# Kernel tuning notes

Hardware: AMD Instinct MI355X
Metric: run time of the kernel (lower is better)

Reference implementation:

```python
import jax, jax.numpy as jnp
import numpy as np

TIME_SHIFT_OFFSET = 288
NOTE_OFF_OFFSET = 128
VELOCITY_OFFSET = 256
MAX_REL_POS = 25
MAX_REL_TIME = 200
MAX_REL_PITCH = 128


def _last_true_pos(flag):
    # flag: (B,T) bool -> (B,T) index of most recent True at or before each position, -1 if none
    B, T = flag.shape
    pos = jnp.where(flag, jnp.arange(T)[None, :], -1)
    return jax.lax.cummax(pos, axis=1)


def time_rel_idx(tok):
    # Faithful vectorization of Head.relative_time index computation.
    B, T = tok.shape
    is_t = tok >= TIME_SHIFT_OFFSET
    vals = jnp.where(is_t, tok - TIME_SHIFT_OFFSET, 0)
    abs_t = (jnp.cumsum(vals, axis=1) + 1).astype(jnp.float32)
    last = _last_true_pos(is_t)
    cur = jnp.where(last >= 0, jnp.take_along_axis(abs_t, jnp.maximum(last, 0), axis=1), jnp.nan)
    prop = jnp.round(cur / 10.0)  # (B,T), NaN before first time token
    dist = prop[:, None, :] - prop[:, :, None]  # [b,i,j] = prop[j]-prop[i]
    idx = jnp.clip(dist, -MAX_REL_TIME, MAX_REL_TIME) + MAX_REL_TIME
    return jnp.where(jnp.isnan(idx), 0.0, idx).astype(jnp.int32)  # (B,T,T)


def pitch_rel_idx(tok):
    # Per the reference loop, note values are also written one step ahead (i-1,i,i+1),
    # so position j ends up with the note value known after step min(j+1, T-1).
    B, T = tok.shape
    is_n = tok < VELOCITY_OFFSET
    vals = (jnp.where(tok >= NOTE_OFF_OFFSET, tok - NOTE_OFF_OFFSET, tok) + 1).astype(jnp.float32)
    last = _last_true_pos(is_n)
    ff = jnp.where(last >= 0, jnp.take_along_axis(vals, jnp.maximum(last, 0), axis=1), jnp.nan)
    prop = ff[:, jnp.minimum(jnp.arange(T) + 1, T - 1)]
    dist = prop[:, None, :] - prop[:, :, None]
    idx = jnp.clip(dist, -MAX_REL_PITCH, MAX_REL_PITCH) + MAX_REL_PITCH
    return jnp.where(jnp.isnan(idx), 0.0, idx).astype(jnp.int32)  # (B,T,T)


def setup_inputs() -> dict:
    key = jax.random.key(0)
    ks = jax.random.split(key, 12)
    B, T, C, H = 2, 512, 512, 64
    x = jax.random.normal(ks[0], (B, T, C), dtype=jnp.float32)
    token_batch = jax.random.randint(ks[1], (B, T), 0, 388)
    s = C ** -0.5
    Wk = jax.random.normal(ks[2], (C, H), dtype=jnp.float32) * s
    Wq = jax.random.normal(ks[3], (C, H), dtype=jnp.float32) * s
    Wv = jax.random.normal(ks[4], (C, H), dtype=jnp.float32) * s
    e = 0.02
    Ek_pos = jax.random.normal(ks[5], (2 * MAX_REL_POS + 1, H), dtype=jnp.float32) * e
    Ev_pos = jax.random.normal(ks[6], (2 * MAX_REL_POS + 1, H), dtype=jnp.float32) * e
    Ek_time = jax.random.normal(ks[7], (2 * MAX_REL_TIME + 1, H), dtype=jnp.float32) * e
    Ev_time = jax.random.normal(ks[8], (2 * MAX_REL_TIME + 1, H), dtype=jnp.float32) * e
    Ek_pitch = jax.random.normal(ks[9], (2 * MAX_REL_PITCH + 1, H), dtype=jnp.float32) * e
    Ev_pitch = jax.random.normal(ks[10], (2 * MAX_REL_PITCH + 1, H), dtype=jnp.float32) * e
    return dict(x=x, token_batch=token_batch, Wk=Wk, Wq=Wq, Wv=Wv,
                Ek_pos=Ek_pos, Ev_pos=Ev_pos, Ek_time=Ek_time, Ev_time=Ev_time,
                Ek_pitch=Ek_pitch, Ev_pitch=Ev_pitch)


def reference(x, token_batch, Wk, Wq, Wv, Ek_pos, Ev_pos, Ek_time, Ev_time, Ek_pitch, Ev_pitch):
    B, T, C = x.shape
    q = x @ Wq  # (B,T,H)
    k = x @ Wk
    v = x @ Wv
    wei = jnp.einsum('btc,bsc->bts', q, k) * (C ** -0.5)  # (B,T,T), scaled by n_embd per source
    pos = jnp.arange(T)
    pd = jnp.clip(pos[None, :] - pos[:, None], -MAX_REL_POS, MAX_REL_POS) + MAX_REL_POS  # (T,T)
    tidx = time_rel_idx(token_batch)
    nidx = pitch_rel_idx(token_batch)
    # Note: the source einsums sum the relative embeddings over i as well (btj output).
    wei = wei + jnp.einsum('ijc,btc->btj', Ek_pos[pd], q)
    wei = wei + jnp.einsum('bijc,btc->btj', Ek_time[tidx], q)
    wei = wei + jnp.einsum('bijc,btc->btj', Ek_pitch[nidx], q)
    causal = jnp.tril(jnp.ones((T, T), dtype=bool))
    wei = jnp.where(causal[None], wei, -jnp.inf)
    wei = jax.nn.softmax(wei, axis=-1)  # dropout p=0.0
    out = wei @ v
    out = out + jnp.einsum('ijc,btj->btc', Ev_pos[pd], wei)
    out = out + jnp.einsum('bijc,btj->btc', Ev_time[tidx], wei)
    out = out + jnp.einsum('bijc,btj->btc', Ev_pitch[nidx], wei)
    return out
```

## Files before the change

### kernel.cpp

```cpp
#include <hip/hip_runtime.h>
#include <math.h>

#define B 2
#define T 512
#define C 512
#define H 64

#define SCALE 0.044194173824159216f

static __device__ __forceinline__ float qnan() { return __builtin_nanf(""); }

__global__ __launch_bounds__(64) void scan_kernel(const int* __restrict__ tok,
                                                  float* __restrict__ prop_t,
                                                  float* __restrict__ prop_p,
                                                  int* __restrict__ cntP,
                                                  int* __restrict__ meta,
                                                  float* __restrict__ tval,
                                                  int* __restrict__ tcnt) {
    int b = blockIdx.x;
    int lane = threadIdx.x;
    const int* tb = tok + b * T;

    __shared__ int tks[T];
    __shared__ float ptv[T];
    __shared__ float ff[T];
    __shared__ int hist[129];
    __shared__ int cnts[520];
    __shared__ int nanPc;

    for (int i = lane; i < T; i += 64) tks[i] = tb[i];
    for (int i = lane; i < 520; i += 64) cnts[i] = 0;
    for (int i = lane; i < 129; i += 64) hist[i] = 0;
    if (lane == 0) nanPc = 0;
    __syncthreads();

    const int p0 = lane * 8;
    unsigned long long lowmask = lane ? ((1ull << lane) - 1ull) : 0ull;

    {
        float lsum[8];
        bool lflag[8];
        float s = 0.f;
        bool f = false;
#pragma unroll
        for (int i = 0; i < 8; ++i) {
            int tk = tks[p0 + i];
            if (tk >= 288) { s += (float)(tk - 288); f = true; }
            lsum[i] = s;
            lflag[i] = f;
        }
        float inc = s;
#pragma unroll
        for (int off = 1; off < 64; off <<= 1) {
            float o = __shfl_up(inc, off);
            if (lane >= off) inc += o;
        }
        float ex = inc - s;
        unsigned long long fmask = __ballot(f);
        bool exf = (fmask & lowmask) != 0ull;
#pragma unroll
        for (int i = 0; i < 8; ++i) {
            bool have = exf | lflag[i];
            float outv = have ? rintf((ex + lsum[i] + 1.0f) / 10.0f) : qnan();
            prop_t[b * T + p0 + i] = outv;
            ptv[p0 + i] = outv;
        }
    }

    {
        float lval[8];
        bool lvalid[8];
        float cv = 0.f;
        bool cvd = false;
#pragma unroll
        for (int i = 0; i < 8; ++i) {
            int tk = tks[p0 + i];
            if (tk < 256) {
                cv = (float)((tk >= 128 ? tk - 128 : tk) + 1);
                cvd = true;
            }
            lval[i] = cv;
            lvalid[i] = cvd;
        }
        unsigned long long vmask = __ballot(cvd);
        unsigned long long lower = vmask & lowmask;
        bool exvd = lower != 0ull;
        int src = 63 - __clzll(lower | 1ull);
        float exv = __shfl(cv, src);
#pragma unroll
        for (int i = 0; i < 8; ++i) {
            bool hv = exvd | lvalid[i];
            float fv = lvalid[i] ? lval[i] : exv;
            ff[p0 + i] = hv ? fv : qnan();
        }
    }
    __syncthreads();

    for (int i = lane; i < T; i += 64) {
        float v = ff[min(i + 1, T - 1)];
        prop_p[b * T + i] = v;
        if (v == v) atomicAdd(&hist[(int)v - 1], 1);
        else atomicAdd(&nanPc, 1);
    }

    int lstart[8];
    int lcnt = 0, lnan = 0;
#pragma unroll
    for (int u = 0; u < 8; ++u) {
        int i = p0 + u;
        float cur = ptv[i];
        bool val = (cur == cur);
        bool st = false;
        if (val) {
            if (i == 0) st = true;
            else {
                float pv = ptv[i - 1];
                st = !(pv == pv) || (pv != cur);
            }
        } else lnan++;
        lstart[u] = st;
        lcnt += st;
    }
    int incs = lcnt;
#pragma unroll
    for (int off = 1; off < 64; off <<= 1) {
        int o = __shfl_up(incs, off);
        if (lane >= off) incs += o;
    }
    int base = incs - lcnt;
    int Lruns = __shfl(incs, 63);
    int tn = lnan;
#pragma unroll
    for (int off = 32; off; off >>= 1) tn += __shfl_down(tn, off);
    tn = __shfl(tn, 0);

    int s2 = base;
#pragma unroll
    for (int u = 0; u < 8; ++u) {
        int i = p0 + u;
        float cur = ptv[i];
        if (lstart[u]) { tval[b * 520 + s2] = cur; s2++; }
        if (cur == cur) atomicAdd(&cnts[s2 - 1], 1);
    }
    __syncthreads();

    for (int i = lane; i < Lruns; i += 64) tcnt[b * 520 + i] = cnts[i];
    for (int i = lane; i < 129; i += 64) cntP[b * 129 + i] = hist[i];
    if (lane == 0) {
        meta[b * 4] = Lruns;
        meta[b * 4 + 1] = tn;
        meta[b * 4 + 2] = nanPc;
    }
}

__global__ __launch_bounds__(256) void qkv_kernel(const float* __restrict__ x,
                                                  const float* __restrict__ Wq,
                                                  const float* __restrict__ Wk,
                                                  const float* __restrict__ Wv,
                                                  float* __restrict__ q,
                                                  float* __restrict__ k,
                                                  float* __restrict__ v) {
    int rg = blockIdx.x & 63;
    int m = blockIdx.x >> 6;
    int tid = threadIdx.x;
    int wave = tid >> 6;
    int lane = tid & 63;
    int g = lane >> 4;
    int c4 = lane & 15;

    const float* Wm = (m == 0) ? Wq : ((m == 1) ? Wk : Wv);
    float* Om = (m == 0) ? q : ((m == 1) ? k : v);

    __shared__ float xs[16 * C];
    const float4* xv4 = (const float4*)(x + (size_t)rg * 16 * C);
    float4* xs4 = (float4*)xs;
#pragma unroll
    for (int i = 0; i < 8; ++i) xs4[tid + 256 * i] = xv4[tid + 256 * i];
    __syncthreads();

    const float4* W4 = (const float4*)Wm;
    const float* xr = xs + (wave * 4) * C;

    float4 a0 = make_float4(0.f, 0.f, 0.f, 0.f);
    float4 a1 = a0, a2 = a0, a3 = a0;
#pragma unroll 4
    for (int u = 0; u < 128; ++u) {
        int kk = u * 4 + g;
        float4 w4 = W4[kk * 16 + c4];
        float x0 = xr[kk];
        float x1 = xr[C + kk];
        float x2 = xr[2 * C + kk];
        float x3 = xr[3 * C + kk];
        a0.x = fmaf(x0, w4.x, a0.x); a0.y = fmaf(x0, w4.y, a0.y);
        a0.z = fmaf(x0, w4.z, a0.z); a0.w = fmaf(x0, w4.w, a0.w);
        a1.x = fmaf(x1, w4.x, a1.x); a1.y = fmaf(x1, w4.y, a1.y);
        a1.z = fmaf(x1, w4.z, a1.z); a1.w = fmaf(x1, w4.w, a1.w);
        a2.x = fmaf(x2, w4.x, a2.x); a2.y = fmaf(x2, w4.y, a2.y);
        a2.z = fmaf(x2, w4.z, a2.z); a2.w = fmaf(x2, w4.w, a2.w);
        a3.x = fmaf(x3, w4.x, a3.x); a3.y = fmaf(x3, w4.y, a3.y);
        a3.z = fmaf(x3, w4.z, a3.z); a3.w = fmaf(x3, w4.w, a3.w);
    }

#pragma unroll
    for (int mask = 16; mask <= 32; mask <<= 1) {
        a0.x += __shfl_xor(a0.x, mask); a0.y += __shfl_xor(a0.y, mask);
        a0.z += __shfl_xor(a0.z, mask); a0.w += __shfl_xor(a0.w, mask);
        a1.x += __shfl_xor(a1.x, mask); a1.y += __shfl_xor(a1.y, mask);
        a1.z += __shfl_xor(a1.z, mask); a1.w += __shfl_xor(a1.w, mask);
        a2.x += __shfl_xor(a2.x, mask); a2.y += __shfl_xor(a2.y, mask);
        a2.z += __shfl_xor(a2.z, mask); a2.w += __shfl_xor(a2.w, mask);
        a3.x += __shfl_xor(a3.x, mask); a3.y += __shfl_xor(a3.y, mask);
        a3.z += __shfl_xor(a3.z, mask); a3.w += __shfl_xor(a3.w, mask);
    }

    if (g == 0) {
        size_t row0 = (size_t)(rg * 16 + wave * 4);
        ((float4*)(Om + (row0 + 0) * H))[c4] = a0;
        ((float4*)(Om + (row0 + 1) * H))[c4] = a1;
        ((float4*)(Om + (row0 + 2) * H))[c4] = a2;
        ((float4*)(Om + (row0 + 3) * H))[c4] = a3;
    }
}

__global__ __launch_bounds__(256) void relsum_kernel(
    const float* __restrict__ prop_t, const float* __restrict__ prop_p,
    const int* __restrict__ cntP, const int* __restrict__ meta,
    const float* __restrict__ tval, const int* __restrict__ tcnt,
    const float* __restrict__ Ek_pos, const float* __restrict__ Ev_pos,
    const float* __restrict__ Ek_time, const float* __restrict__ Ev_time,
    const float* __restrict__ Ek_pitch, const float* __restrict__ Ev_pitch,
    float* __restrict__ k, float* __restrict__ v) {
    int b = blockIdx.x >> 9;
    int j = blockIdx.x & 511;
    int tid = threadIdx.x;
    int wave = tid >> 6;
    int c = tid & 63;

    __shared__ float tvL[520];
    __shared__ int tcL[520];
    __shared__ int cpL[132];
    __shared__ float redK[256];
    __shared__ float redV[256];

    int L = meta[b * 4];
    int nanT = meta[b * 4 + 1];
    int nanP = meta[b * 4 + 2];
    for (int i = tid; i < L; i += 256) {
        tvL[i] = tval[b * 520 + i];
        tcL[i] = tcnt[b * 520 + i];
    }
    if (tid < 129) cpL[tid] = cntP[b * 129 + tid];
    else if (tid < 132) cpL[tid] = 0;
    __syncthreads();

    float pjt = prop_t[b * T + j];
    float pjp = prop_p[b * T + j];
    bool pvalid = (pjp == pjp);
    int ipjp = pvalid ? (int)pjp : 0;

    float aK = 0.f, aV = 0.f;

#pragma unroll 3
    for (int i = 0; i < 33; ++i) {
        int e = wave + i * 4;
        int cnt = cpL[e];
        if (cnt) {
            int idx = pvalid ? (ipjp + 127 - e) : 0;
            float fc = (float)cnt;
            aK = fmaf(fc, Ek_pitch[idx * H + c], aK);
            aV = fmaf(fc, Ev_pitch[idx * H + c], aV);
        }
    }
    if (wave == 3 && nanP) {
        float fc = (float)nanP;
        aK = fmaf(fc, Ek_pitch[c], aK);
        aV = fmaf(fc, Ev_pitch[c], aV);
    }

#pragma unroll 2
    for (int r = wave; r < L; r += 4) {
        int cnt = tcL[r];
        float dt = pjt - tvL[r];
        int idx = (dt != dt) ? 0 : (int)fminf(fmaxf(dt, -200.f), 200.f) + 200;
        float fc = (float)cnt;
        aK = fmaf(fc, Ek_time[idx * H + c], aK);
        aV = fmaf(fc, Ev_time[idx * H + c], aV);
    }
    if (wave == 1 && nanT) {
        float fc = (float)nanT;
        aK = fmaf(fc, Ek_time[c], aK);
        aV = fmaf(fc, Ev_time[c], aV);
    }

    int lo = max(-25, j - (T - 1));
    int hi = min(25, j);
    for (int d = lo + wave; d <= hi; d += 4) {
        aK += Ek_pos[(d + 25) * H + c];
        aV += Ev_pos[(d + 25) * H + c];
    }
    if (wave == 0) {
        float c50 = (float)max(j - 25, 0);
        float c0 = (float)max((T - 26) - j, 0);
        aK = fmaf(c50, Ek_pos[50 * H + c], aK);
        aK = fmaf(c0, Ek_pos[0 * H + c], aK);
        aV = fmaf(c50, Ev_pos[50 * H + c], aV);
        aV = fmaf(c0, Ev_pos[0 * H + c], aV);
    }

    redK[tid] = aK;
    redV[tid] = aV;
    __syncthreads();

    if (tid < 64) {
        float sK = redK[tid] + redK[64 + tid] + redK[128 + tid] + redK[192 + tid];
        float sV = redV[tid] + redV[64 + tid] + redV[128 + tid] + redV[192 + tid];
        size_t o = (size_t)blockIdx.x * H + tid;
        k[o] = SCALE * k[o] + sK;
        v[o] = v[o] + sV;
    }
}

__global__ __launch_bounds__(256) void attn_kernel(const float* __restrict__ q,
                                                   const float* __restrict__ kp,
                                                   const float* __restrict__ vp,
                                                   float* __restrict__ out) {
    int b = blockIdx.x >> 7;
    int g = blockIdx.x & 127;
    int tid = threadIdx.x;
    int wave = tid >> 6;
    int lane = tid & 63;

    int t = (wave < 2) ? (2 * g + wave) : (511 - 2 * g - (wave - 2));
    int ns = t + 1;

    __shared__ float kt[64 * 65];
    __shared__ float vt[64 * 64];
    __shared__ float qs[4][64];
    __shared__ float pS[4][64];

    qs[wave][lane] = q[((size_t)b * T + t) * H + lane];

    const float* kb = kp + (size_t)b * T * H;
    const float* vb = vp + (size_t)b * T * H;
    int ntiles = (512 - 2 * g + 63) / 64;

    float m = -INFINITY;
    float l = 0.f;
    float acc = 0.f;

    for (int it = 0; it < ntiles; ++it) {
        int s0 = it * 64;

#pragma unroll
        for (int i = 0; i < 4; ++i) {
            int f = i * 256 + tid;
            int r = f >> 4;
            int c0 = (f & 15) << 2;
            int sr = min(s0 + r, T - 1);
            const float4 kv = *(const float4*)(kb + (size_t)sr * H + c0);
            const float4 vv = *(const float4*)(vb + (size_t)sr * H + c0);
            kt[r * 65 + c0 + 0] = kv.x;
            kt[r * 65 + c0 + 1] = kv.y;
            kt[r * 65 + c0 + 2] = kv.z;
            kt[r * 65 + c0 + 3] = kv.w;
            *(float4*)(vt + r * 64 + c0) = vv;
        }
        __syncthreads();

        if (s0 < ns) {
            int s = s0 + lane;
            float sc = -INFINITY;
            if (s < ns) {
                const float* kr = kt + lane * 65;
                const float* qw = qs[wave];
                float d0 = 0.f, d1 = 0.f, d2 = 0.f, d3 = 0.f;
#pragma unroll
                for (int c = 0; c < 64; c += 4) {
                    d0 = fmaf(qw[c + 0], kr[c + 0], d0);
                    d1 = fmaf(qw[c + 1], kr[c + 1], d1);
                    d2 = fmaf(qw[c + 2], kr[c + 2], d2);
                    d3 = fmaf(qw[c + 3], kr[c + 3], d3);
                }
                sc = (d0 + d1) + (d2 + d3);
            }
            float mt = sc;
#pragma unroll
            for (int off = 32; off; off >>= 1) mt = fmaxf(mt, __shfl_xor(mt, off));
            float mnew = fmaxf(m, mt);
            float alpha = __expf(m - mnew);
            float p = (s < ns) ? __expf(sc - mnew) : 0.f;
            l = l * alpha + p;
            pS[wave][lane] = p;
            m = mnew;

            float a0 = 0.f, a1 = 0.f, a2 = 0.f, a3 = 0.f;
            int smax = min(64, ns - s0);
            const float* pw = pS[wave];
            int ss = 0;
            for (; ss + 4 <= smax; ss += 4) {
                a0 = fmaf(pw[ss + 0], vt[(ss + 0) * 64 + lane], a0);
                a1 = fmaf(pw[ss + 1], vt[(ss + 1) * 64 + lane], a1);
                a2 = fmaf(pw[ss + 2], vt[(ss + 2) * 64 + lane], a2);
                a3 = fmaf(pw[ss + 3], vt[(ss + 3) * 64 + lane], a3);
            }
            for (; ss < smax; ++ss)
                a0 = fmaf(pw[ss], vt[ss * 64 + lane], a0);
            acc = acc * alpha + ((a0 + a1) + (a2 + a3));
        }
        __syncthreads();
    }

    float lt = l;
#pragma unroll
    for (int off = 32; off; off >>= 1) lt += __shfl_xor(lt, off);

    out[((size_t)b * T + t) * H + lane] = acc / lt;
}

extern "C" void kernel_launch(void* const* d_in, const int* in_sizes, int n_in,
                              void* d_out, int out_size, void* d_ws, size_t ws_size,
                              hipStream_t stream) {
    const float* x        = (const float*)d_in[0];
    const int*   tok      = (const int*)d_in[1];
    const float* Wk       = (const float*)d_in[2];
    const float* Wq       = (const float*)d_in[3];
    const float* Wv       = (const float*)d_in[4];
    const float* Ek_pos   = (const float*)d_in[5];
    const float* Ev_pos   = (const float*)d_in[6];
    const float* Ek_time  = (const float*)d_in[7];
    const float* Ev_time  = (const float*)d_in[8];
    const float* Ek_pitch = (const float*)d_in[9];
    const float* Ev_pitch = (const float*)d_in[10];
    float* out = (float*)d_out;

    float* ws = (float*)d_ws;
    float* q      = ws;
    float* k      = q + B * T * H;
    float* v      = k + B * T * H;
    float* prop_t = v + B * T * H;
    float* prop_p = prop_t + B * T;
    int*   cntP   = (int*)(prop_p + B * T);
    int*   meta   = cntP + B * 129;
    float* tval   = (float*)(meta + B * 4);
    int*   tcnt   = (int*)(tval + B * 520);

    scan_kernel<<<B, 64, 0, stream>>>(tok, prop_t, prop_p, cntP, meta, tval, tcnt);
    qkv_kernel<<<3 * 64, 256, 0, stream>>>(x, Wq, Wk, Wv, q, k, v);
    relsum_kernel<<<B * T, 256, 0, stream>>>(prop_t, prop_p, cntP, meta, tval, tcnt,
                                             Ek_pos, Ev_pos, Ek_time, Ev_time,
                                             Ek_pitch, Ev_pitch, k, v);
    attn_kernel<<<B * 128, 256, 0, stream>>>(q, k, v, out);
}
```

Baseline: 131.0 us.

## Fuse token scan, QKV projection and relative-sum into one kernel

Merges three kernels (scan, qkv, relsum) into a single kernel of 256 blocks. Each block handles 4 rows: wave 0 redoes the per-batch token scan in shared memory, and waves 1-3 compute the q, k and v projections for those rows. After a barrier, each wave does the relative-embedding sum for one row with no cross-wave reduction. This removes two launches and the global round-trips for intermediates, but every block repeats the scan redundantly and each wave now walks the full pitch and time loops serially.

```diff
diff --git a/kernel.cpp b/kernel.cpp
--- a/kernel.cpp
+++ b/kernel.cpp
@@ -10,314 +10,279 @@
 
 static __device__ __forceinline__ float qnan() { return __builtin_nanf(""); }
 
-__global__ __launch_bounds__(64) void scan_kernel(const int* __restrict__ tok,
-                                                  float* __restrict__ prop_t,
-                                                  float* __restrict__ prop_p,
-                                                  int* __restrict__ cntP,
-                                                  int* __restrict__ meta,
-                                                  float* __restrict__ tval,
-                                                  int* __restrict__ tcnt) {
-    int b = blockIdx.x;
-    int lane = threadIdx.x;
-    const int* tb = tok + b * T;
-
-    __shared__ int tks[T];
-    __shared__ float ptv[T];
-    __shared__ float ff[T];
-    __shared__ int hist[129];
-    __shared__ int cnts[520];
-    __shared__ int nanPc;
-
-    for (int i = lane; i < T; i += 64) tks[i] = tb[i];
-    for (int i = lane; i < 520; i += 64) cnts[i] = 0;
-    for (int i = lane; i < 129; i += 64) hist[i] = 0;
-    if (lane == 0) nanPc = 0;
-    __syncthreads();
-
-    const int p0 = lane * 8;
-    unsigned long long lowmask = lane ? ((1ull << lane) - 1ull) : 0ull;
-
-    {
-        float lsum[8];
-        bool lflag[8];
-        float s = 0.f;
-        bool f = false;
-#pragma unroll
-        for (int i = 0; i < 8; ++i) {
-            int tk = tks[p0 + i];
-            if (tk >= 288) { s += (float)(tk - 288); f = true; }
-            lsum[i] = s;
-            lflag[i] = f;
-        }
-        float inc = s;
-#pragma unroll
-        for (int off = 1; off < 64; off <<= 1) {
-            float o = __shfl_up(inc, off);
-            if (lane >= off) inc += o;
-        }
-        float ex = inc - s;
-        unsigned long long fmask = __ballot(f);
-        bool exf = (fmask & lowmask) != 0ull;
-#pragma unroll
-        for (int i = 0; i < 8; ++i) {
-            bool have = exf | lflag[i];
-            float outv = have ? rintf((ex + lsum[i] + 1.0f) / 10.0f) : qnan();
-            prop_t[b * T + p0 + i] = outv;
-            ptv[p0 + i] = outv;
-        }
-    }
-
-    {
-        float lval[8];
-        bool lvalid[8];
-        float cv = 0.f;
-        bool cvd = false;
-#pragma unroll
-        for (int i = 0; i < 8; ++i) {
-            int tk = tks[p0 + i];
-            if (tk < 256) {
-                cv = (float)((tk >= 128 ? tk - 128 : tk) + 1);
-                cvd = true;
-            }
-            lval[i] = cv;
-            lvalid[i] = cvd;
-        }
-        unsigned long long vmask = __ballot(cvd);
-        unsigned long long lower = vmask & lowmask;
-        bool exvd = lower != 0ull;
-        int src = 63 - __clzll(lower | 1ull);
-        float exv = __shfl(cv, src);
-#pragma unroll
-        for (int i = 0; i < 8; ++i) {
-            bool hv = exvd | lvalid[i];
-            float fv = lvalid[i] ? lval[i] : exv;
-            ff[p0 + i] = hv ? fv : qnan();
-        }
-    }
-    __syncthreads();
-
-    for (int i = lane; i < T; i += 64) {
-        float v = ff[min(i + 1, T - 1)];
-        prop_p[b * T + i] = v;
-        if (v == v) atomicAdd(&hist[(int)v - 1], 1);
-        else atomicAdd(&nanPc, 1);
-    }
-
-    int lstart[8];
-    int lcnt = 0, lnan = 0;
-#pragma unroll
-    for (int u = 0; u < 8; ++u) {
-        int i = p0 + u;
-        float cur = ptv[i];
-        bool val = (cur == cur);
-        bool st = false;
-        if (val) {
-            if (i == 0) st = true;
-            else {
-                float pv = ptv[i - 1];
-                st = !(pv == pv) || (pv != cur);
-            }
-        } else lnan++;
-        lstart[u] = st;
-        lcnt += st;
-    }
-    int incs = lcnt;
-#pragma unroll
-    for (int off = 1; off < 64; off <<= 1) {
-        int o = __shfl_up(incs, off);
-        if (lane >= off) incs += o;
-    }
-    int base = incs - lcnt;
-    int Lruns = __shfl(incs, 63);
-    int tn = lnan;
-#pragma unroll
-    for (int off = 32; off; off >>= 1) tn += __shfl_down(tn, off);
-    tn = __shfl(tn, 0);
-
-    int s2 = base;
-#pragma unroll
-    for (int u = 0; u < 8; ++u) {
-        int i = p0 + u;
-        float cur = ptv[i];
-        if (lstart[u]) { tval[b * 520 + s2] = cur; s2++; }
-        if (cur == cur) atomicAdd(&cnts[s2 - 1], 1);
-    }
-    __syncthreads();
-
-    for (int i = lane; i < Lruns; i += 64) tcnt[b * 520 + i] = cnts[i];
-    for (int i = lane; i < 129; i += 64) cntP[b * 129 + i] = hist[i];
-    if (lane == 0) {
-        meta[b * 4] = Lruns;
-        meta[b * 4 + 1] = tn;
-        meta[b * 4 + 2] = nanPc;
-    }
-}
-
-__global__ __launch_bounds__(256) void qkv_kernel(const float* __restrict__ x,
-                                                  const float* __restrict__ Wq,
-                                                  const float* __restrict__ Wk,
-                                                  const float* __restrict__ Wv,
-                                                  float* __restrict__ q,
-                                                  float* __restrict__ k,
-                                                  float* __restrict__ v) {
-    int rg = blockIdx.x & 63;
-    int m = blockIdx.x >> 6;
+__global__ __launch_bounds__(256) void fused_kernel(
+    const int* __restrict__ tok, const float* __restrict__ x,
+    const float* __restrict__ Wq, const float* __restrict__ Wk,
+    const float* __restrict__ Wv,
+    const float* __restrict__ Ek_pos, const float* __restrict__ Ev_pos,
+    const float* __restrict__ Ek_time, const float* __restrict__ Ev_time,
+    const float* __restrict__ Ek_pitch, const float* __restrict__ Ev_pitch,
+    float* __restrict__ q, float* __restrict__ k, float* __restrict__ v) {
+    int bid = blockIdx.x;
+    int b = bid >> 7;
+    int j0 = (bid & 127) * 4;
     int tid = threadIdx.x;
     int wave = tid >> 6;
     int lane = tid & 63;
-    int g = lane >> 4;
-    int c4 = lane & 15;
-
-    const float* Wm = (m == 0) ? Wq : ((m == 1) ? Wk : Wv);
-    float* Om = (m == 0) ? q : ((m == 1) ? k : v);
-
-    __shared__ float xs[16 * C];
-    const float4* xv4 = (const float4*)(x + (size_t)rg * 16 * C);
-    float4* xs4 = (float4*)xs;
-#pragma unroll
-    for (int i = 0; i < 8; ++i) xs4[tid + 256 * i] = xv4[tid + 256 * i];
+
+    __shared__ int   tks[T];
+    __shared__ float ptv[T];
+    __shared__ float ppv[T];
+    __shared__ float tvalL[520];
+    __shared__ int   cnts[520];
+    __shared__ int   hist[129];
+    __shared__ int   metaL[2];
+    __shared__ int   nanPc;
+    __shared__ float xs[4 * C];
+    __shared__ float kvK[4][64];
+    __shared__ float kvV[4][64];
+
+    {
+        const int* tb = tok + b * T;
+        tks[tid] = tb[tid];
+        tks[tid + 256] = tb[tid + 256];
+        const float4* xv4 = (const float4*)(x + (size_t)(b * T + j0) * C);
+        float4* xs4 = (float4*)xs;
+        xs4[tid] = xv4[tid];
+        xs4[tid + 256] = xv4[tid + 256];
+        for (int i = tid; i < 520; i += 256) cnts[i] = 0;
+        if (tid < 129) hist[tid] = 0;
+        if (tid == 255) nanPc = 0;
+    }
     __syncthreads();
 
-    const float4* W4 = (const float4*)Wm;
-    const float* xr = xs + (wave * 4) * C;
-
-    float4 a0 = make_float4(0.f, 0.f, 0.f, 0.f);
-    float4 a1 = a0, a2 = a0, a3 = a0;
+    if (wave == 0) {
+        const int p0 = lane * 8;
+        unsigned long long lowmask = lane ? ((1ull << lane) - 1ull) : 0ull;
+
+        float tv[8];
+        {
+            float lsum[8];
+            bool lflag[8];
+            float s = 0.f;
+            bool f = false;
+#pragma unroll
+            for (int u = 0; u < 8; ++u) {
+                int tk = tks[p0 + u];
+                if (tk >= 288) { s += (float)(tk - 288); f = true; }
+                lsum[u] = s;
+                lflag[u] = f;
+            }
+            float inc = s;
+#pragma unroll
+            for (int off = 1; off < 64; off <<= 1) {
+                float o = __shfl_up(inc, off);
+                if (lane >= off) inc += o;
+            }
+            float ex = inc - s;
+            unsigned long long fmask = __ballot(f);
+            bool exf = (fmask & lowmask) != 0ull;
+#pragma unroll
+            for (int u = 0; u < 8; ++u) {
+                bool have = exf | lflag[u];
+                tv[u] = have ? rintf((ex + lsum[u] + 1.0f) / 10.0f) : qnan();
+                ptv[p0 + u] = tv[u];
+            }
+        }
+
+        float fv[8];
+        {
+            bool lvalid[8];
+            float cv = 0.f;
+            bool cvd = false;
+#pragma unroll
+            for (int u = 0; u < 8; ++u) {
+                int tk = tks[p0 + u];
+                if (tk < 256) {
+                    cv = (float)((tk >= 128 ? tk - 128 : tk) + 1);
+                    cvd = true;
+                }
+                fv[u] = cv;
+                lvalid[u] = cvd;
+            }
+            unsigned long long vmask = __ballot(cvd);
+            unsigned long long lower = vmask & lowmask;
+            bool exvd = lower != 0ull;
+            int src = 63 - __clzll(lower | 1ull);
+            float exv = __shfl(cv, src);
+#pragma unroll
+            for (int u = 0; u < 8; ++u) {
+                bool hv = exvd | lvalid[u];
+                fv[u] = lvalid[u] ? fv[u] : exv;
+                fv[u] = hv ? fv[u] : qnan();
+            }
+        }
+
+        {
+            float nf0 = __shfl_down(fv[0], 1);
+#pragma unroll
+            for (int u = 0; u < 8; ++u) {
+                float sv = (u < 7) ? fv[u + 1] : ((lane == 63) ? fv[7] : nf0);
+                ppv[p0 + u] = sv;
+                if (sv == sv) atomicAdd(&hist[(int)sv - 1], 1);
+                else atomicAdd(&nanPc, 1);
+            }
+        }
+
+        {
+            float pl7 = __shfl_up(tv[7], 1);
+            int lstart[8];
+            int lcnt = 0, lnan = 0;
+#pragma unroll
+            for (int u = 0; u < 8; ++u) {
+                float cur = tv[u];
+                bool val = (cur == cur);
+                float pv = (u > 0) ? tv[u - 1] : pl7;
+                bool st = false;
+                if (val) {
+                    if (p0 + u == 0) st = true;
+                    else st = !(pv == pv) || (pv != cur);
+                } else lnan++;
+                lstart[u] = st;
+                lcnt += st;
+            }
+            int incs = lcnt;
+#pragma unroll
+            for (int off = 1; off < 64; off <<= 1) {
+                int o = __shfl_up(incs, off);
+                if (lane >= off) incs += o;
+            }
+            int base = incs - lcnt;
+            int Lruns = __shfl(incs, 63);
+            int tn = lnan;
+#pragma unroll
+            for (int off = 32; off; off >>= 1) tn += __shfl_down(tn, off);
+            tn = __shfl(tn, 0);
+
+            int s2 = base;
+#pragma unroll
+            for (int u = 0; u < 8; ++u) {
+                float cur = tv[u];
+                if (lstart[u]) { tvalL[s2] = cur; s2++; }
+                if (cur == cur) atomicAdd(&cnts[s2 - 1], 1);
+            }
+            if (lane == 0) { metaL[0] = Lruns; metaL[1] = tn; }
+        }
+    } else {
+        int m = wave - 1;
+        const float* Wm = (m == 0) ? Wq : ((m == 1) ? Wk : Wv);
+        int g = lane >> 4;
+        int c4 = lane & 15;
+        const float4* W4 = (const float4*)Wm;
+
+        float4 a0 = make_float4(0.f, 0.f, 0.f, 0.f);
+        float4 a1 = a0, a2 = a0, a3 = a0;
 #pragma unroll 4
-    for (int u = 0; u < 128; ++u) {
-        int kk = u * 4 + g;
-        float4 w4 = W4[kk * 16 + c4];
-        float x0 = xr[kk];
-        float x1 = xr[C + kk];
-        float x2 = xr[2 * C + kk];
-        float x3 = xr[3 * C + kk];
-        a0.x = fmaf(x0, w4.x, a0.x); a0.y = fmaf(x0, w4.y, a0.y);
-        a0.z = fmaf(x0, w4.z, a0.z); a0.w = fmaf(x0, w4.w, a0.w);
-        a1.x = fmaf(x1, w4.x, a1.x); a1.y = fmaf(x1, w4.y, a1.y);
-        a1.z = fmaf(x1, w4.z, a1.z); a1.w = fmaf(x1, w4.w, a1.w);
-        a2.x = fmaf(x2, w4.x, a2.x); a2.y = fmaf(x2, w4.y, a2.y);
-        a2.z = fmaf(x2, w4.z, a2.z); a2.w = fmaf(x2, w4.w, a2.w);
-        a3.x = fmaf(x3, w4.x, a3.x); a3.y = fmaf(x3, w4.y, a3.y);
-        a3.z = fmaf(x3, w4.z, a3.z); a3.w = fmaf(x3, w4.w, a3.w);
-    }
-
-#pragma unroll
-    for (int mask = 16; mask <= 32; mask <<= 1) {
-        a0.x += __shfl_xor(a0.x, mask); a0.y += __shfl_xor(a0.y, mask);
-        a0.z += __shfl_xor(a0.z, mask); a0.w += __shfl_xor(a0.w, mask);
-        a1.x += __shfl_xor(a1.x, mask); a1.y += __shfl_xor(a1.y, mask);
-        a1.z += __shfl_xor(a1.z, mask); a1.w += __shfl_xor(a1.w, mask);
-        a2.x += __shfl_xor(a2.x, mask); a2.y += __shfl_xor(a2.y, mask);
-        a2.z += __shfl_xor(a2.z, mask); a2.w += __shfl_xor(a2.w, mask);
-        a3.x += __shfl_xor(a3.x, mask); a3.y += __shfl_xor(a3.y, mask);
-        a3.z += __shfl_xor(a3.z, mask); a3.w += __shfl_xor(a3.w, mask);
-    }
-
-    if (g == 0) {
-        size_t row0 = (size_t)(rg * 16 + wave * 4);
-        ((float4*)(Om + (row0 + 0) * H))[c4] = a0;
-        ((float4*)(Om + (row0 + 1) * H))[c4] = a1;
-        ((float4*)(Om + (row0 + 2) * H))[c4] = a2;
-        ((float4*)(Om + (row0 + 3) * H))[c4] = a3;
-    }
-}
-
-__global__ __launch_bounds__(256) void relsum_kernel(
-    const float* __restrict__ prop_t, const float* __restrict__ prop_p,
-    const int* __restrict__ cntP, const int* __restrict__ meta,
-    const float* __restrict__ tval, const int* __restrict__ tcnt,
-    const float* __restrict__ Ek_pos, const float* __restrict__ Ev_pos,
-    const float* __restrict__ Ek_time, const float* __restrict__ Ev_time,
-    const float* __restrict__ Ek_pitch, const float* __restrict__ Ev_pitch,
-    float* __restrict__ k, float* __restrict__ v) {
-    int b = blockIdx.x >> 9;
-    int j = blockIdx.x & 511;
-    int tid = threadIdx.x;
-    int wave = tid >> 6;
-    int c = tid & 63;
-
-    __shared__ float tvL[520];
-    __shared__ int tcL[520];
-    __shared__ int cpL[132];
-    __shared__ float redK[256];
-    __shared__ float redV[256];
-
-    int L = meta[b * 4];
-    int nanT = meta[b * 4 + 1];
-    int nanP = meta[b * 4 + 2];
-    for (int i = tid; i < L; i += 256) {
-        tvL[i] = tval[b * 520 + i];
-        tcL[i] = tcnt[b * 520 + i];
-    }
-    if (tid < 129) cpL[tid] = cntP[b * 129 + tid];
-    else if (tid < 132) cpL[tid] = 0;
+        for (int u = 0; u < 128; ++u) {
+            int kk = u * 4 + g;
+            float4 w4 = W4[kk * 16 + c4];
+            float x0 = xs[kk];
+            float x1 = xs[C + kk];
+            float x2 = xs[2 * C + kk];
+            float x3 = xs[3 * C + kk];
+            a0.x = fmaf(x0, w4.x, a0.x); a0.y = fmaf(x0, w4.y, a0.y);
+            a0.z = fmaf(x0, w4.z, a0.z); a0.w = fmaf(x0, w4.w, a0.w);
+            a1.x = fmaf(x1, w4.x, a1.x); a1.y = fmaf(x1, w4.y, a1.y);
+            a1.z = fmaf(x1, w4.z, a1.z); a1.w = fmaf(x1, w4.w, a1.w);
+            a2.x = fmaf(x2, w4.x, a2.x); a2.y = fmaf(x2, w4.y, a2.y);
+            a2.z = fmaf(x2, w4.z, a2.z); a2.w = fmaf(x2, w4.w, a2.w);
+            a3.x = fmaf(x3, w4.x, a3.x); a3.y = fmaf(x3, w4.y, a3.y);
+            a3.z = fmaf(x3, w4.z, a3.z); a3.w = fmaf(x3, w4.w, a3.w);
+        }
+#pragma unroll
+        for (int mask = 16; mask <= 32; mask <<= 1) {
+            a0.x += __shfl_xor(a0.x, mask); a0.y += __shfl_xor(a0.y, mask);
+            a0.z += __shfl_xor(a0.z, mask); a0.w += __shfl_xor(a0.w, mask);
+            a1.x += __shfl_xor(a1.x, mask); a1.y += __shfl_xor(a1.y, mask);
+            a1.z += __shfl_xor(a1.z, mask); a1.w += __shfl_xor(a1.w, mask);
+            a2.x += __shfl_xor(a2.x, mask); a2.y += __shfl_xor(a2.y, mask);
+            a2.z += __shfl_xor(a2.z, mask); a2.w += __shfl_xor(a2.w, mask);
+            a3.x += __shfl_xor(a3.x, mask); a3.y += __shfl_xor(a3.y, mask);
+            a3.z += __shfl_xor(a3.z, mask); a3.w += __shfl_xor(a3.w, mask);
+        }
+        if (g == 0) {
+            if (m == 0) {
+                size_t r0 = (size_t)(b * T + j0);
+                ((float4*)(q + (r0 + 0) * H))[c4] = a0;
+                ((float4*)(q + (r0 + 1) * H))[c4] = a1;
+                ((float4*)(q + (r0 + 2) * H))[c4] = a2;
+                ((float4*)(q + (r0 + 3) * H))[c4] = a3;
+            } else if (m == 1) {
+                ((float4*)&kvK[0][0])[c4] = a0;
+                ((float4*)&kvK[1][0])[c4] = a1;
+                ((float4*)&kvK[2][0])[c4] = a2;
+                ((float4*)&kvK[3][0])[c4] = a3;
+            } else {
+                ((float4*)&kvV[0][0])[c4] = a0;
+                ((float4*)&kvV[1][0])[c4] = a1;
+                ((float4*)&kvV[2][0])[c4] = a2;
+                ((float4*)&kvV[3][0])[c4] = a3;
+            }
+        }
+    }
     __syncthreads();
 
-    float pjt = prop_t[b * T + j];
-    float pjp = prop_p[b * T + j];
+    int j = j0 + wave;
+    int L = metaL[0];
+    int nanT = metaL[1];
+    int nanP = nanPc;
+    float pjt = ptv[j];
+    float pjp = ppv[j];
     bool pvalid = (pjp == pjp);
     int ipjp = pvalid ? (int)pjp : 0;
 
     float aK = 0.f, aV = 0.f;
 
-#pragma unroll 3
-    for (int i = 0; i < 33; ++i) {
-        int e = wave + i * 4;
-        int cnt = cpL[e];
+#pragma unroll 4
+    for (int e = 0; e < 129; ++e) {
+        int cnt = hist[e];
         if (cnt) {
             int idx = pvalid ? (ipjp + 127 - e) : 0;
             float fc = (float)cnt;
-            aK = fmaf(fc, Ek_pitch[idx * H + c], aK);
-            aV = fmaf(fc, Ev_pitch[idx * H + c], aV);
-        }
-    }
-    if (wave == 3 && nanP) {
+            aK = fmaf(fc, Ek_pitch[idx * H + lane], aK);
+            aV = fmaf(fc, Ev_pitch[idx * H + lane], aV);
+        }
+    }
+    if (nanP) {
         float fc = (float)nanP;
-        aK = fmaf(fc, Ek_pitch[c], aK);
-        aV = fmaf(fc, Ev_pitch[c], aV);
+        aK = fmaf(fc, Ek_pitch[lane], aK);
+        aV = fmaf(fc, Ev_pitch[lane], aV);
     }
 
 #pragma unroll 2
-    for (int r = wave; r < L; r += 4) {
-        int cnt = tcL[r];
-        float dt = pjt - tvL[r];
+    for (int r = 0; r < L; ++r) {
+        int cnt = cnts[r];
+        float dt = pjt - tvalL[r];
         int idx = (dt != dt) ? 0 : (int)fminf(fmaxf(dt, -200.f), 200.f) + 200;
         float fc = (float)cnt;
-        aK = fmaf(fc, Ek_time[idx * H + c], aK);
-        aV = fmaf(fc, Ev_time[idx * H + c], aV);
-    }
-    if (wave == 1 && nanT) {
+        aK = fmaf(fc, Ek_time[idx * H + lane], aK);
+        aV = fmaf(fc, Ev_time[idx * H + lane], aV);
+    }
+    if (nanT) {
         float fc = (float)nanT;
-        aK = fmaf(fc, Ek_time[c], aK);
-        aV = fmaf(fc, Ev_time[c], aV);
+        aK = fmaf(fc, Ek_time[lane], aK);
+        aV = fmaf(fc, Ev_time[lane], aV);
     }
 
     int lo = max(-25, j - (T - 1));
     int hi = min(25, j);
-    for (int d = lo + wave; d <= hi; d += 4) {
-        aK += Ek_pos[(d + 25) * H + c];
-        aV += Ev_pos[(d + 25) * H + c];
-    }
-    if (wave == 0) {
+#pragma unroll 4
+    for (int d = lo; d <= hi; ++d) {
+        aK += Ek_pos[(d + 25) * H + lane];
+        aV += Ev_pos[(d + 25) * H + lane];
+    }
+    {
         float c50 = (float)max(j - 25, 0);
         float c0 = (float)max((T - 26) - j, 0);
-        aK = fmaf(c50, Ek_pos[50 * H + c], aK);
-        aK = fmaf(c0, Ek_pos[0 * H + c], aK);
-        aV = fmaf(c50, Ev_pos[50 * H + c], aV);
-        aV = fmaf(c0, Ev_pos[0 * H + c], aV);
-    }
-
-    redK[tid] = aK;
-    redV[tid] = aV;
-    __syncthreads();
-
-    if (tid < 64) {
-        float sK = redK[tid] + redK[64 + tid] + redK[128 + tid] + redK[192 + tid];
-        float sV = redV[tid] + redV[64 + tid] + redV[128 + tid] + redV[192 + tid];
-        size_t o = (size_t)blockIdx.x * H + tid;
-        k[o] = SCALE * k[o] + sK;
-        v[o] = v[o] + sV;
-    }
+        aK = fmaf(c50, Ek_pos[50 * H + lane], aK);
+        aK = fmaf(c0, Ek_pos[0 * H + lane], aK);
+        aV = fmaf(c50, Ev_pos[50 * H + lane], aV);
+        aV = fmaf(c0, Ev_pos[0 * H + lane], aV);
+    }
+
+    size_t o = (size_t)(b * T + j) * H + lane;
+    k[o] = SCALE * kvK[wave][lane] + aK;
+    v[o] = kvV[wave][lane] + aV;
 }
 
 __global__ __launch_bounds__(256) void attn_kernel(const float* __restrict__ q,
@@ -434,20 +399,12 @@
     float* out = (float*)d_out;
 
     float* ws = (float*)d_ws;
-    float* q      = ws;
-    float* k      = q + B * T * H;
-    float* v      = k + B * T * H;
-    float* prop_t = v + B * T * H;
-    float* prop_p = prop_t + B * T;
-    int*   cntP   = (int*)(prop_p + B * T);
-    int*   meta   = cntP + B * 129;
-    float* tval   = (float*)(meta + B * 4);
-    int*   tcnt   = (int*)(tval + B * 520);
-
-    scan_kernel<<<B, 64, 0, stream>>>(tok, prop_t, prop_p, cntP, meta, tval, tcnt);
-    qkv_kernel<<<3 * 64, 256, 0, stream>>>(x, Wq, Wk, Wv, q, k, v);
-    relsum_kernel<<<B * T, 256, 0, stream>>>(prop_t, prop_p, cntP, meta, tval, tcnt,
-                                             Ek_pos, Ev_pos, Ek_time, Ev_time,
-                                             Ek_pitch, Ev_pitch, k, v);
+    float* q = ws;
+    float* k = q + B * T * H;
+    float* v = k + B * T * H;
+
+    fused_kernel<<<B * 128, 256, 0, stream>>>(tok, x, Wq, Wk, Wv,
+                                              Ek_pos, Ev_pos, Ek_time, Ev_time,
+                                              Ek_pitch, Ev_pitch, q, k, v);
     attn_kernel<<<B * 128, 256, 0, stream>>>(q, k, v, out);
 }
```

After: 151.4 us. 15.6% more time.

## Fuse scan into QKV kernel and split attention rows across wave pairs

Applied to the files above, without the earlier changes.

Merges the token-scan kernel into the QKV projection launch as two extra blocks, which removes one kernel launch. The scan now keeps its values in registers and uses shuffles instead of shared-memory staging. The attention kernel now gives each block two query rows instead of four. Each row is handled by a pair of waves that take alternating key tiles, and their partial softmax states are merged at the end. This doubles the block count and the parallelism per row, at the cost of more K/V tile loads per output row and an extra merge step.

```diff
diff --git a/kernel.cpp b/kernel.cpp
--- a/kernel.cpp
+++ b/kernel.cpp
@@ -10,44 +10,110 @@
 
 static __device__ __forceinline__ float qnan() { return __builtin_nanf(""); }
 
-__global__ __launch_bounds__(64) void scan_kernel(const int* __restrict__ tok,
-                                                  float* __restrict__ prop_t,
-                                                  float* __restrict__ prop_p,
-                                                  int* __restrict__ cntP,
-                                                  int* __restrict__ meta,
-                                                  float* __restrict__ tval,
-                                                  int* __restrict__ tcnt) {
-    int b = blockIdx.x;
-    int lane = threadIdx.x;
-    const int* tb = tok + b * T;
-
-    __shared__ int tks[T];
-    __shared__ float ptv[T];
-    __shared__ float ff[T];
-    __shared__ int hist[129];
-    __shared__ int cnts[520];
-    __shared__ int nanPc;
-
-    for (int i = lane; i < T; i += 64) tks[i] = tb[i];
-    for (int i = lane; i < 520; i += 64) cnts[i] = 0;
-    for (int i = lane; i < 129; i += 64) hist[i] = 0;
-    if (lane == 0) nanPc = 0;
+__global__ __launch_bounds__(256) void qkv_scan_kernel(
+    const float* __restrict__ x, const int* __restrict__ tok,
+    const float* __restrict__ Wq, const float* __restrict__ Wk,
+    const float* __restrict__ Wv,
+    float* __restrict__ q, float* __restrict__ k, float* __restrict__ v,
+    float* __restrict__ prop_t, float* __restrict__ prop_p,
+    int* __restrict__ cntP, int* __restrict__ meta,
+    float* __restrict__ tval, int* __restrict__ tcnt) {
+    int bid = blockIdx.x;
+    int tid = threadIdx.x;
+    int wave = tid >> 6;
+    int lane = tid & 63;
+
+    __shared__ float xs[16 * C];
+    __shared__ int   tks[T];
+    __shared__ int   cnts[520];
+    __shared__ int   hist[129];
+    __shared__ int   nanPc;
+
+    if (bid < 192) {
+        int rg = bid & 63;
+        int m = bid >> 6;
+        int g = lane >> 4;
+        int c4 = lane & 15;
+
+        const float* Wm = (m == 0) ? Wq : ((m == 1) ? Wk : Wv);
+        float* Om = (m == 0) ? q : ((m == 1) ? k : v);
+
+        const float4* xv4 = (const float4*)(x + (size_t)rg * 16 * C);
+        float4* xs4 = (float4*)xs;
+#pragma unroll
+        for (int i = 0; i < 8; ++i) xs4[tid + 256 * i] = xv4[tid + 256 * i];
+        __syncthreads();
+
+        const float4* W4 = (const float4*)Wm;
+        const float* xr = xs + (wave * 4) * C;
+
+        float4 a0 = make_float4(0.f, 0.f, 0.f, 0.f);
+        float4 a1 = a0, a2 = a0, a3 = a0;
+#pragma unroll 4
+        for (int u = 0; u < 128; ++u) {
+            int kk = u * 4 + g;
+            float4 w4 = W4[kk * 16 + c4];
+            float x0 = xr[kk];
+            float x1 = xr[C + kk];
+            float x2 = xr[2 * C + kk];
+            float x3 = xr[3 * C + kk];
+            a0.x = fmaf(x0, w4.x, a0.x); a0.y = fmaf(x0, w4.y, a0.y);
+            a0.z = fmaf(x0, w4.z, a0.z); a0.w = fmaf(x0, w4.w, a0.w);
+            a1.x = fmaf(x1, w4.x, a1.x); a1.y = fmaf(x1, w4.y, a1.y);
+            a1.z = fmaf(x1, w4.z, a1.z); a1.w = fmaf(x1, w4.w, a1.w);
+            a2.x = fmaf(x2, w4.x, a2.x); a2.y = fmaf(x2, w4.y, a2.y);
+            a2.z = fmaf(x2, w4.z, a2.z); a2.w = fmaf(x2, w4.w, a2.w);
+            a3.x = fmaf(x3, w4.x, a3.x); a3.y = fmaf(x3, w4.y, a3.y);
+            a3.z = fmaf(x3, w4.z, a3.z); a3.w = fmaf(x3, w4.w, a3.w);
+        }
+#pragma unroll
+        for (int mask = 16; mask <= 32; mask <<= 1) {
+            a0.x += __shfl_xor(a0.x, mask); a0.y += __shfl_xor(a0.y, mask);
+            a0.z += __shfl_xor(a0.z, mask); a0.w += __shfl_xor(a0.w, mask);
+            a1.x += __shfl_xor(a1.x, mask); a1.y += __shfl_xor(a1.y, mask);
+            a1.z += __shfl_xor(a1.z, mask); a1.w += __shfl_xor(a1.w, mask);
+            a2.x += __shfl_xor(a2.x, mask); a2.y += __shfl_xor(a2.y, mask);
+            a2.z += __shfl_xor(a2.z, mask); a2.w += __shfl_xor(a2.w, mask);
+            a3.x += __shfl_xor(a3.x, mask); a3.y += __shfl_xor(a3.y, mask);
+            a3.z += __shfl_xor(a3.z, mask); a3.w += __shfl_xor(a3.w, mask);
+        }
+        if (g == 0) {
+            size_t row0 = (size_t)(rg * 16 + wave * 4);
+            ((float4*)(Om + (row0 + 0) * H))[c4] = a0;
+            ((float4*)(Om + (row0 + 1) * H))[c4] = a1;
+            ((float4*)(Om + (row0 + 2) * H))[c4] = a2;
+            ((float4*)(Om + (row0 + 3) * H))[c4] = a3;
+        }
+        return;
+    }
+
+    int b = bid - 192;
+    {
+        const int* tb = tok + b * T;
+        tks[tid] = tb[tid];
+        tks[tid + 256] = tb[tid + 256];
+        for (int i = tid; i < 520; i += 256) cnts[i] = 0;
+        if (tid < 129) hist[tid] = 0;
+        if (tid == 255) nanPc = 0;
+    }
     __syncthreads();
+    if (wave != 0) return;
 
     const int p0 = lane * 8;
     unsigned long long lowmask = lane ? ((1ull << lane) - 1ull) : 0ull;
 
+    float tv[8];
     {
         float lsum[8];
         bool lflag[8];
         float s = 0.f;
         bool f = false;
 #pragma unroll
-        for (int i = 0; i < 8; ++i) {
-            int tk = tks[p0 + i];
+        for (int u = 0; u < 8; ++u) {
+            int tk = tks[p0 + u];
             if (tk >= 288) { s += (float)(tk - 288); f = true; }
-            lsum[i] = s;
-            lflag[i] = f;
+            lsum[u] = s;
+            lflag[u] = f;
         }
         float inc = s;
 #pragma unroll
@@ -59,28 +125,27 @@
         unsigned long long fmask = __ballot(f);
         bool exf = (fmask & lowmask) != 0ull;
 #pragma unroll
-        for (int i = 0; i < 8; ++i) {
-            bool have = exf | lflag[i];
-            float outv = have ? rintf((ex + lsum[i] + 1.0f) / 10.0f) : qnan();
-            prop_t[b * T + p0 + i] = outv;
-            ptv[p0 + i] = outv;
-        }
-    }
-
+        for (int u = 0; u < 8; ++u) {
+            bool have = exf | lflag[u];
+            tv[u] = have ? rintf((ex + lsum[u] + 1.0f) / 10.0f) : qnan();
+            prop_t[b * T + p0 + u] = tv[u];
+        }
+    }
+
+    float fv[8];
     {
-        float lval[8];
         bool lvalid[8];
         float cv = 0.f;
         bool cvd = false;
 #pragma unroll
-        for (int i = 0; i < 8; ++i) {
-            int tk = tks[p0 + i];
+        for (int u = 0; u < 8; ++u) {
+            int tk = tks[p0 + u];
             if (tk < 256) {
                 cv = (float)((tk >= 128 ? tk - 128 : tk) + 1);
                 cvd = true;
             }
-            lval[i] = cv;
-            lvalid[i] = cvd;
+            fv[u] = cv;
+            lvalid[u] = cvd;
         }
         unsigned long long vmask = __ballot(cvd);
         unsigned long long lower = vmask & lowmask;
@@ -88,137 +153,68 @@
         int src = 63 - __clzll(lower | 1ull);
         float exv = __shfl(cv, src);
 #pragma unroll
-        for (int i = 0; i < 8; ++i) {
-            bool hv = exvd | lvalid[i];
-            float fv = lvalid[i] ? lval[i] : exv;
-            ff[p0 + i] = hv ? fv : qnan();
-        }
-    }
-    __syncthreads();
-
-    for (int i = lane; i < T; i += 64) {
-        float v = ff[min(i + 1, T - 1)];
-        prop_p[b * T + i] = v;
-        if (v == v) atomicAdd(&hist[(int)v - 1], 1);
-        else atomicAdd(&nanPc, 1);
-    }
-
-    int lstart[8];
-    int lcnt = 0, lnan = 0;
-#pragma unroll
-    for (int u = 0; u < 8; ++u) {
-        int i = p0 + u;
-        float cur = ptv[i];
-        bool val = (cur == cur);
-        bool st = false;
-        if (val) {
-            if (i == 0) st = true;
-            else {
-                float pv = ptv[i - 1];
-                st = !(pv == pv) || (pv != cur);
-            }
-        } else lnan++;
-        lstart[u] = st;
-        lcnt += st;
-    }
-    int incs = lcnt;
-#pragma unroll
-    for (int off = 1; off < 64; off <<= 1) {
-        int o = __shfl_up(incs, off);
-        if (lane >= off) incs += o;
-    }
-    int base = incs - lcnt;
-    int Lruns = __shfl(incs, 63);
-    int tn = lnan;
-#pragma unroll
-    for (int off = 32; off; off >>= 1) tn += __shfl_down(tn, off);
-    tn = __shfl(tn, 0);
-
-    int s2 = base;
-#pragma unroll
-    for (int u = 0; u < 8; ++u) {
-        int i = p0 + u;
-        float cur = ptv[i];
-        if (lstart[u]) { tval[b * 520 + s2] = cur; s2++; }
-        if (cur == cur) atomicAdd(&cnts[s2 - 1], 1);
-    }
-    __syncthreads();
-
-    for (int i = lane; i < Lruns; i += 64) tcnt[b * 520 + i] = cnts[i];
-    for (int i = lane; i < 129; i += 64) cntP[b * 129 + i] = hist[i];
-    if (lane == 0) {
-        meta[b * 4] = Lruns;
-        meta[b * 4 + 1] = tn;
-        meta[b * 4 + 2] = nanPc;
-    }
-}
-
-__global__ __launch_bounds__(256) void qkv_kernel(const float* __restrict__ x,
-                                                  const float* __restrict__ Wq,
-                                                  const float* __restrict__ Wk,
-                                                  const float* __restrict__ Wv,
-                                                  float* __restrict__ q,
-                                                  float* __restrict__ k,
-                                                  float* __restrict__ v) {
-    int rg = blockIdx.x & 63;
-    int m = blockIdx.x >> 6;
-    int tid = threadIdx.x;
-    int wave = tid >> 6;
-    int lane = tid & 63;
-    int g = lane >> 4;
-    int c4 = lane & 15;
-
-    const float* Wm = (m == 0) ? Wq : ((m == 1) ? Wk : Wv);
-    float* Om = (m == 0) ? q : ((m == 1) ? k : v);
-
-    __shared__ float xs[16 * C];
-    const float4* xv4 = (const float4*)(x + (size_t)rg * 16 * C);
-    float4* xs4 = (float4*)xs;
-#pragma unroll
-    for (int i = 0; i < 8; ++i) xs4[tid + 256 * i] = xv4[tid + 256 * i];
-    __syncthreads();
-
-    const float4* W4 = (const float4*)Wm;
-    const float* xr = xs + (wave * 4) * C;
-
-    float4 a0 = make_float4(0.f, 0.f, 0.f, 0.f);
-    float4 a1 = a0, a2 = a0, a3 = a0;
-#pragma unroll 4
-    for (int u = 0; u < 128; ++u) {
-        int kk = u * 4 + g;
-        float4 w4 = W4[kk * 16 + c4];
-        float x0 = xr[kk];
-        float x1 = xr[C + kk];
-        float x2 = xr[2 * C + kk];
-        float x3 = xr[3 * C + kk];
-        a0.x = fmaf(x0, w4.x, a0.x); a0.y = fmaf(x0, w4.y, a0.y);
-        a0.z = fmaf(x0, w4.z, a0.z); a0.w = fmaf(x0, w4.w, a0.w);
-        a1.x = fmaf(x1, w4.x, a1.x); a1.y = fmaf(x1, w4.y, a1.y);
-        a1.z = fmaf(x1, w4.z, a1.z); a1.w = fmaf(x1, w4.w, a1.w);
-        a2.x = fmaf(x2, w4.x, a2.x); a2.y = fmaf(x2, w4.y, a2.y);
-        a2.z = fmaf(x2, w4.z, a2.z); a2.w = fmaf(x2, w4.w, a2.w);
-        a3.x = fmaf(x3, w4.x, a3.x); a3.y = fmaf(x3, w4.y, a3.y);
-        a3.z = fmaf(x3, w4.z, a3.z); a3.w = fmaf(x3, w4.w, a3.w);
-    }
-
-#pragma unroll
-    for (int mask = 16; mask <= 32; mask <<= 1) {
-        a0.x += __shfl_xor(a0.x, mask); a0.y += __shfl_xor(a0.y, mask);
-        a0.z += __shfl_xor(a0.z, mask); a0.w += __shfl_xor(a0.w, mask);
-        a1.x += __shfl_xor(a1.x, mask); a1.y += __shfl_xor(a1.y, mask);
-        a1.z += __shfl_xor(a1.z, mask); a1.w += __shfl_xor(a1.w, mask);
-        a2.x += __shfl_xor(a2.x, mask); a2.y += __shfl_xor(a2.y, mask);
-        a2.z += __shfl_xor(a2.z, mask); a2.w += __shfl_xor(a2.w, mask);
-        a3.x += __shfl_xor(a3.x, mask); a3.y += __shfl_xor(a3.y, mask);
-        a3.z += __shfl_xor(a3.z, mask); a3.w += __shfl_xor(a3.w, mask);
-    }
-
-    if (g == 0) {
-        size_t row0 = (size_t)(rg * 16 + wave * 4);
-        ((float4*)(Om + (row0 + 0) * H))[c4] = a0;
-        ((float4*)(Om + (row0 + 1) * H))[c4] = a1;
-        ((float4*)(Om + (row0 + 2) * H))[c4] = a2;
-        ((float4*)(Om + (row0 + 3) * H))[c4] = a3;
+        for (int u = 0; u < 8; ++u) {
+            bool hv = exvd | lvalid[u];
+            fv[u] = lvalid[u] ? fv[u] : exv;
+            fv[u] = hv ? fv[u] : qnan();
+        }
+    }
+
+    {
+        float nf0 = __shfl_down(fv[0], 1);
+#pragma unroll
+        for (int u = 0; u < 8; ++u) {
+            float sv = (u < 7) ? fv[u + 1] : ((lane == 63) ? fv[7] : nf0);
+            prop_p[b * T + p0 + u] = sv;
+            if (sv == sv) atomicAdd(&hist[(int)sv - 1], 1);
+            else atomicAdd(&nanPc, 1);
+        }
+    }
+
+    {
+        float pl7 = __shfl_up(tv[7], 1);
+        int lstart[8];
+        int lcnt = 0, lnan = 0;
+#pragma unroll
+        for (int u = 0; u < 8; ++u) {
+            float cur = tv[u];
+            bool val = (cur == cur);
+            float pv = (u > 0) ? tv[u - 1] : pl7;
+            bool st = false;
+            if (val) {
+                if (p0 + u == 0) st = true;
+                else st = !(pv == pv) || (pv != cur);
+            } else lnan++;
+            lstart[u] = st;
+            lcnt += st;
+        }
+        int incs = lcnt;
+#pragma unroll
+        for (int off = 1; off < 64; off <<= 1) {
+            int o = __shfl_up(incs, off);
+            if (lane >= off) incs += o;
+        }
+        int base = incs - lcnt;
+        int Lruns = __shfl(incs, 63);
+        int tn = lnan;
+#pragma unroll
+        for (int off = 32; off; off >>= 1) tn += __shfl_down(tn, off);
+        tn = __shfl(tn, 0);
+
+        int s2 = base;
+#pragma unroll
+        for (int u = 0; u < 8; ++u) {
+            float cur = tv[u];
+            if (lstart[u]) { tval[b * 520 + s2] = cur; s2++; }
+            if (cur == cur) atomicAdd(&cnts[s2 - 1], 1);
+        }
+        for (int i = lane; i < Lruns; i += 64) tcnt[b * 520 + i] = cnts[i];
+        for (int i = lane; i < 129; i += 64) cntP[b * 129 + i] = hist[i];
+        if (lane == 0) {
+            meta[b * 4] = Lruns;
+            meta[b * 4 + 1] = tn;
+        }
+        if (lane == 1) meta[b * 4 + 2] = nanPc;
     }
 }
 
@@ -324,29 +320,35 @@
                                                    const float* __restrict__ kp,
                                                    const float* __restrict__ vp,
                                                    float* __restrict__ out) {
-    int b = blockIdx.x >> 7;
-    int g = blockIdx.x & 127;
+    int b = blockIdx.x >> 8;
+    int g = blockIdx.x & 255;
     int tid = threadIdx.x;
     int wave = tid >> 6;
     int lane = tid & 63;
 
-    int t = (wave < 2) ? (2 * g + wave) : (511 - 2 * g - (wave - 2));
-    int ns = t + 1;
+    int row = (wave < 2) ? g : (511 - g);
+    int ns = row + 1;
+    int nw = (ns + 63) >> 6;
+    int par = wave & 1;
 
     __shared__ float kt[64 * 65];
     __shared__ float vt[64 * 64];
-    __shared__ float qs[4][64];
+    __shared__ float qs[2][64];
     __shared__ float pS[4][64];
-
-    qs[wave][lane] = q[((size_t)b * T + t) * H + lane];
+    __shared__ float mM[4], lM[4];
+    __shared__ float accM[4][64];
+
+    if (wave == 0) qs[0][lane] = q[((size_t)b * T + g) * H + lane];
+    if (wave == 2) qs[1][lane] = q[((size_t)b * T + 511 - g) * H + lane];
 
     const float* kb = kp + (size_t)b * T * H;
     const float* vb = vp + (size_t)b * T * H;
-    int ntiles = (512 - 2 * g + 63) / 64;
+    int ntiles = (512 - g + 63) >> 6;
 
     float m = -INFINITY;
     float l = 0.f;
     float acc = 0.f;
+    const float* qw = qs[wave >> 1];
 
     for (int it = 0; it < ntiles; ++it) {
         int s0 = it * 64;
@@ -367,12 +369,11 @@
         }
         __syncthreads();
 
-        if (s0 < ns) {
+        if (it < nw && (it & 1) == par) {
             int s = s0 + lane;
             float sc = -INFINITY;
             if (s < ns) {
                 const float* kr = kt + lane * 65;
-                const float* qw = qs[wave];
                 float d0 = 0.f, d1 = 0.f, d2 = 0.f, d3 = 0.f;
 #pragma unroll
                 for (int c = 0; c < 64; c += 4) {
@@ -413,8 +414,21 @@
     float lt = l;
 #pragma unroll
     for (int off = 32; off; off >>= 1) lt += __shfl_xor(lt, off);
-
-    out[((size_t)b * T + t) * H + lane] = acc / lt;
+    mM[wave] = m;
+    lM[wave] = lt;
+    accM[wave][lane] = acc;
+    __syncthreads();
+
+    if ((wave & 1) == 0) {
+        int w1 = wave | 1;
+        float m0 = mM[wave], m1 = mM[w1];
+        float m12 = fmaxf(m0, m1);
+        float al0 = __expf(m0 - m12);
+        float al1 = __expf(m1 - m12);
+        float lsum = lM[wave] * al0 + lM[w1] * al1;
+        float o = (accM[wave][lane] * al0 + accM[w1][lane] * al1) / lsum;
+        out[((size_t)b * T + row) * H + lane] = o;
+    }
 }
 
 extern "C" void kernel_launch(void* const* d_in, const int* in_sizes, int n_in,
@@ -444,10 +458,11 @@
     float* tval   = (float*)(meta + B * 4);
     int*   tcnt   = (int*)(tval + B * 520);
 
-    scan_kernel<<<B, 64, 0, stream>>>(tok, prop_t, prop_p, cntP, meta, tval, tcnt);
-    qkv_kernel<<<3 * 64, 256, 0, stream>>>(x, Wq, Wk, Wv, q, k, v);
+    qkv_scan_kernel<<<192 + B, 256, 0, stream>>>(x, tok, Wq, Wk, Wv, q, k, v,
+                                                 prop_t, prop_p, cntP, meta,
+                                                 tval, tcnt);
     relsum_kernel<<<B * T, 256, 0, stream>>>(prop_t, prop_p, cntP, meta, tval, tcnt,
                                              Ek_pos, Ev_pos, Ek_time, Ev_time,
                                              Ek_pitch, Ev_pitch, k, v);
-    attn_kernel<<<B * 128, 256, 0, stream>>>(q, k, v, out);
+    attn_kernel<<<B * 256, 256, 0, stream>>>(q, k, v, out);
 }
```

After: 124.8 us. 1.05x faster.
